# Performance work log

Measured on AMD Instinct MI355X. Metric: run time of the kernel, lower is better.

## Reference

```python
import jax, jax.numpy as jnp
import numpy as np

WS = 8   # window_size
SS = 4   # shift_size
NH = 12  # num_heads
DIM = 384
HD = DIM // NH


def _rel_index():
    coords = np.stack(np.meshgrid(np.arange(WS), np.arange(WS), indexing='ij'))  # (2, ws, ws)
    cf = coords.reshape(2, -1)                       # (2, n)
    rel = (cf[:, :, None] - cf[:, None, :]).transpose(1, 2, 0).copy()  # (n, n, 2)
    rel[..., 0] += WS - 1
    rel[..., 1] += WS - 1
    rel[..., 0] *= 2 * WS - 1
    return rel.sum(-1)                               # (n, n) int


def _attn_mask(h, w):
    img = np.zeros((h, w))
    sl = (slice(0, -WS), slice(-WS, -SS), slice(-SS, None))
    cnt = 0
    for hs in sl:
        for ws_ in sl:
            img[hs, ws_] = cnt
            cnt += 1
    mw = img.reshape(h // WS, WS, w // WS, WS).transpose(0, 2, 1, 3).reshape(-1, WS * WS)  # (nW, n)
    d = mw[:, None, :] - mw[:, :, None]
    return np.where(d != 0, -100.0, 0.0).astype(np.float32)  # (nW, n, n)


def setup_inputs() -> dict:
    key = jax.random.key(0)
    ks = jax.random.split(key, 10)
    B, H, W = 32, 64, 64
    std = 0.02
    return {
        'x': jax.random.normal(ks[0], (B, H, W, DIM), jnp.float32),
        'wq': jax.random.normal(ks[1], (DIM, DIM), jnp.float32) * std,
        'bq': jnp.zeros((DIM,), jnp.float32),
        'wk': jax.random.normal(ks[2], (DIM, DIM), jnp.float32) * std,
        'bk': jnp.zeros((DIM,), jnp.float32),
        'wv': jax.random.normal(ks[3], (DIM, DIM), jnp.float32) * std,
        'bv': jnp.zeros((DIM,), jnp.float32),
        'wo': jax.random.normal(ks[4], (DIM, DIM), jnp.float32) * std,
        'bo': jnp.zeros((DIM,), jnp.float32),
        'bias_table': jax.random.normal(ks[5], ((2 * WS - 1) ** 2, NH), jnp.float32) * std,
    }


def reference(x, wq, bq, wk, bk, wv, bv, wo, bo, bias_table):
    b, h, w, c = x.shape
    pad_h = (-h) % WS
    pad_w = (-w) % WS
    if pad_h or pad_w:
        x = jnp.pad(x, ((0, 0), (0, pad_h), (0, pad_w), (0, 0)))
    hp, wp = x.shape[1], x.shape[2]

    if SS > 0:
        x_sh = jnp.roll(x, shift=(-SS, -SS), axis=(1, 2))
        mask = jnp.asarray(_attn_mask(hp, wp))          # (nW, n, n)
    else:
        x_sh = x
        mask = None

    # window partition -> (B*nW, n, C)
    nwh, nww = hp // WS, wp // WS
    win = x_sh.reshape(b, nwh, WS, nww, WS, c).transpose(0, 1, 3, 2, 4, 5)
    win = win.reshape(-1, WS * WS, c)
    b_, n, _ = win.shape

    scale = HD ** -0.5
    q = (win @ wq.T + bq).reshape(b_, n, NH, HD).transpose(0, 2, 1, 3) * scale
    k = (win @ wk.T + bk).reshape(b_, n, NH, HD).transpose(0, 2, 1, 3)
    v = (win @ wv.T + bv).reshape(b_, n, NH, HD).transpose(0, 2, 1, 3)

    attn = jnp.einsum('bhnd,bhmd->bhnm', q, k)          # (b_, NH, n, n)
    rel = bias_table[jnp.asarray(_rel_index()).reshape(-1)].reshape(n, n, NH)
    attn = attn + rel.transpose(2, 0, 1)[None]
    if mask is not None:
        nW = mask.shape[0]
        attn = attn.reshape(b_ // nW, nW, NH, n, n) + mask[None, :, None]
        attn = attn.reshape(b_, NH, n, n)
    attn = jax.nn.softmax(attn, axis=-1)

    out = jnp.einsum('bhnm,bhmd->bhnd', attn, v).transpose(0, 2, 1, 3).reshape(b_, n, c)
    out = out @ wo.T + bo

    # window reverse -> (B, hp, wp, C)
    out = out.reshape(b, nwh, nww, WS, WS, c).transpose(0, 1, 3, 2, 4, 5).reshape(b, hp, wp, c)
    if SS > 0:
        out = jnp.roll(out, shift=(SS, SS), axis=(1, 2))
    return out[:, :h, :w, :]
```

## Files before the change

kernel.cpp:

```cpp
#include <hip/hip_runtime.h>
#include <hip/hip_bf16.h>

typedef short bf16x8 __attribute__((ext_vector_type(8)));
typedef float f32x4 __attribute__((ext_vector_type(4)));

#define NH_ 12
#define DIM_ 384

static __device__ __forceinline__ float bf2f_us(ushort u) {
    __hip_bfloat16 h; __builtin_memcpy(&h, &u, 2);
    return __bfloat162float(h);
}
static __device__ __forceinline__ ushort f2us(float f) {
    __hip_bfloat16 h = __float2bfloat16(f);
    ushort u; __builtin_memcpy(&u, &h, 2);
    return u;
}

static __device__ __forceinline__ void gload_lds16(const void* g, void* l) {
    __builtin_amdgcn_global_load_lds(
        (const __attribute__((address_space(1))) unsigned int*)g,
        (__attribute__((address_space(3))) unsigned int*)l, 16, 0, 0);
}

static __device__ __forceinline__ int regioncnt(int t, int wr, int wc) {
    int rr = (wr == 7) ? (((t >> 3) < 4) ? 1 : 2) : 0;
    int cc = (wc == 7) ? (((t & 7) < 4) ? 1 : 2) : 0;
    return rr * 3 + cc;
}

__global__ __launch_bounds__(256) void convert_kernel(
    const float* wq, const float* wk, const float* wv, const float* wo,
    const float* bq, const float* bk, const float* bv, const float* bo,
    const float* bt, ushort* __restrict__ dst)
{
    const int N = 594060;
    for (int i = blockIdx.x * 256 + threadIdx.x; i < N; i += gridDim.x * 256) {
        const float* src; int off;
        if (i < 589824) {
            int wsel = i / 147456; off = i - wsel * 147456;
            src = (wsel == 0) ? wq : (wsel == 1) ? wk : (wsel == 2) ? wv : wo;
        } else if (i < 591360) {
            int bsel = (i - 589824) / 384; off = (i - 589824) - bsel * 384;
            src = (bsel == 0) ? bq : (bsel == 1) ? bk : (bsel == 2) ? bv : bo;
        } else {
            off = i - 591360; src = bt;
        }
        dst[i] = f2us(src[off]);
    }
}

__global__ void bias_kernel(const ushort* __restrict__ tablec, float* __restrict__ biasmat) {
    int i = blockIdx.x;
    int j = threadIdx.x;
    int idx = ((i >> 3) - (j >> 3) + 7) * 15 + ((i & 7) - (j & 7) + 7);
    #pragma unroll
    for (int h = 0; h < NH_; ++h)
        biasmat[h * 4096 + i * 64 + j] = bf2f_us(tablec[idx * NH_ + h]);
}

__global__ __launch_bounds__(256, 3) void qkv_gemm(
    const float* __restrict__ x, const ushort* __restrict__ wb,
    ushort* __restrict__ qws, ushort* __restrict__ kws, ushort* __restrict__ vws,
    int wbase, int nmb)
{
    __shared__ __align__(16) ushort As[128 * 32];
    __shared__ __align__(16) ushort Bs[128 * 32];
    const int nwg = nmb * 9;
    const int orig = blockIdx.x;
    const int wgid = (orig & 7) * (nwg >> 3) + (orig >> 3);
    const int mb = wgid / 9, nt = wgid - mb * 9;
    const int wsel = nt / 3, ntm = nt - wsel * 3;
    const int n0 = nt * 128;
    const int tid = threadIdx.x, lane = tid & 63, wv = tid >> 6;
    const int col16 = lane & 15, quad = lane >> 4;
    const int wm = wv >> 1, wn = wv & 1;

    const float* arow[4];
    int lrs[4];
    #pragma unroll
    for (int it = 0; it < 4; ++it) {
        const int lr = (tid >> 3) + 32 * it;
        lrs[it] = lr;
        const int wglob = wbase + mb * 2 + (lr >> 6);
        const int token = lr & 63;
        const int b = wglob >> 6, widx = wglob & 63, wr = widx >> 3, wc = widx & 7;
        const int orr = (wr * 8 + (token >> 3) + 4) & 63;
        const int occ = (wc * 8 + (token & 7) + 4) & 63;
        arow[it] = x + (((size_t)b * 64 + orr) * 64 + occ) * DIM_ + (tid & 7) * 4;
    }

    f32x4 acc[4][4];
    #pragma unroll
    for (int i2 = 0; i2 < 4; ++i2)
        #pragma unroll
        for (int j2 = 0; j2 < 4; ++j2)
            acc[i2][j2] = (f32x4){0.f, 0.f, 0.f, 0.f};

    const ushort* bsrc = wb + (size_t)n0 * DIM_;
    const int srow = lane >> 2, scolb = (lane & 3) * 8;

    for (int kk = 0; kk < DIM_; kk += 32) {
        if (kk) __syncthreads();
        #pragma unroll
        for (int c2 = 0; c2 < 2; ++c2) {
            const int row = wv * 32 + c2 * 16 + srow;
            gload_lds16(bsrc + (size_t)row * DIM_ + kk + scolb, Bs + wv * 1024 + c2 * 512);
        }
        #pragma unroll
        for (int it = 0; it < 4; ++it) {
            const float4 v = *reinterpret_cast<const float4*>(arow[it] + kk);
            ushort4 u; u.x = f2us(v.x); u.y = f2us(v.y); u.z = f2us(v.z); u.w = f2us(v.w);
            *reinterpret_cast<ushort4*>(&As[lrs[it] * 32 + (tid & 7) * 4]) = u;
        }
        __syncthreads();
        bf16x8 af[4], bf[4];
        #pragma unroll
        for (int rt = 0; rt < 4; ++rt)
            af[rt] = *reinterpret_cast<const bf16x8*>(&As[(wm * 64 + rt * 16 + col16) * 32 + quad * 8]);
        #pragma unroll
        for (int ct = 0; ct < 4; ++ct)
            bf[ct] = *reinterpret_cast<const bf16x8*>(&Bs[(wn * 64 + ct * 16 + col16) * 32 + quad * 8]);
        #pragma unroll
        for (int rt = 0; rt < 4; ++rt)
            #pragma unroll
            for (int ct = 0; ct < 4; ++ct)
                acc[rt][ct] = __builtin_amdgcn_mfma_f32_16x16x32_bf16(af[rt], bf[ct], acc[rt][ct], 0, 0, 0);
    }

    const int lw = mb * 2 + wm;
    const float scale = 0.17677669529663687f;
    const ushort* bias_all = wb + 589824 + wsel * 384;
    #pragma unroll
    for (int ct = 0; ct < 4; ++ct) {
        const int jl = ntm * 128 + wn * 64 + ct * 16 + col16;
        const int head = jl >> 5, hd = jl & 31;
        const float bj = bf2f_us(bias_all[jl]);
        #pragma unroll
        for (int rt = 0; rt < 4; ++rt) {
            if (wsel == 2) {
                ushort4 pk;
                pk.x = f2us(acc[rt][ct][0] + bj);
                pk.y = f2us(acc[rt][ct][1] + bj);
                pk.z = f2us(acc[rt][ct][2] + bj);
                pk.w = f2us(acc[rt][ct][3] + bj);
                *reinterpret_cast<ushort4*>(
                    vws + ((size_t)(lw * NH_ + head) * 32 + hd) * 64 + rt * 16 + quad * 4) = pk;
            } else {
                #pragma unroll
                for (int r = 0; r < 4; ++r) {
                    const int token = rt * 16 + quad * 4 + r;
                    const float v = acc[rt][ct][r] + bj;
                    if (wsel == 0)
                        qws[((size_t)(lw * NH_ + head) * 64 + token) * 32 + hd] = f2us(v * scale);
                    else
                        kws[((size_t)(lw * NH_ + head) * 64 + token) * 32 + hd] = f2us(v);
                }
            }
        }
    }
}

__global__ __launch_bounds__(64) void attn_kernel(
    const __hip_bfloat16* __restrict__ qws, const __hip_bfloat16* __restrict__ kws,
    const __hip_bfloat16* __restrict__ vws, const float* __restrict__ biasmat,
    __hip_bfloat16* __restrict__ attnout, int wbase)
{
    __shared__ __align__(16) __hip_bfloat16 Pbuf[64 * 72];
    const int bid = blockIdx.x;
    const int lw = bid / NH_, h = bid - lw * NH_;
    const int w = wbase + lw;
    const int lane = threadIdx.x, col16 = lane & 15, quad = lane >> 4;
    const ushort* qp = reinterpret_cast<const ushort*>(qws) + ((size_t)lw * NH_ + h) * 64 * 32;
    const ushort* kp = reinterpret_cast<const ushort*>(kws) + ((size_t)lw * NH_ + h) * 64 * 32;
    const ushort* vp = reinterpret_cast<const ushort*>(vws) + ((size_t)lw * NH_ + h) * 32 * 64;

    bf16x8 aq[4], bk4[4];
    #pragma unroll
    for (int t = 0; t < 4; ++t) {
        aq[t]  = *reinterpret_cast<const bf16x8*>(qp + (t * 16 + col16) * 32 + quad * 8);
        bk4[t] = *reinterpret_cast<const bf16x8*>(kp + (t * 16 + col16) * 32 + quad * 8);
    }
    f32x4 S[4][4];
    #pragma unroll
    for (int rt = 0; rt < 4; ++rt) {
        #pragma unroll
        for (int ct = 0; ct < 4; ++ct) {
            f32x4 z = {0.f,0.f,0.f,0.f};
            S[rt][ct] = __builtin_amdgcn_mfma_f32_16x16x32_bf16(aq[rt], bk4[ct], z, 0, 0, 0);
        }
    }

    const int widx = w & 63, wr = widx >> 3, wc = widx & 7;
    #pragma unroll
    for (int ct = 0; ct < 4; ++ct) {
        const int jj = ct * 16 + col16;
        const int cntj = regioncnt(jj, wr, wc);
        #pragma unroll
        for (int rt = 0; rt < 4; ++rt) {
            #pragma unroll
            for (int r = 0; r < 4; ++r) {
                const int ii = rt * 16 + quad * 4 + r;
                float add = biasmat[h * 4096 + ii * 64 + jj];
                if (regioncnt(ii, wr, wc) != cntj) add -= 100.f;
                S[rt][ct][r] += add;
            }
        }
    }

    #pragma unroll
    for (int rt = 0; rt < 4; ++rt) {
        float rm[4], rs[4];
        #pragma unroll
        for (int r = 0; r < 4; ++r)
            rm[r] = fmaxf(fmaxf(S[rt][0][r], S[rt][1][r]), fmaxf(S[rt][2][r], S[rt][3][r]));
        #pragma unroll
        for (int d = 1; d <= 8; d <<= 1) {
            #pragma unroll
            for (int r = 0; r < 4; ++r) rm[r] = fmaxf(rm[r], __shfl_xor(rm[r], d, 64));
        }
        #pragma unroll
        for (int r = 0; r < 4; ++r) rs[r] = 0.f;
        #pragma unroll
        for (int ct = 0; ct < 4; ++ct) {
            #pragma unroll
            for (int r = 0; r < 4; ++r) {
                float p = __expf(S[rt][ct][r] - rm[r]);
                S[rt][ct][r] = p;
                rs[r] += p;
            }
        }
        #pragma unroll
        for (int d = 1; d <= 8; d <<= 1) {
            #pragma unroll
            for (int r = 0; r < 4; ++r) rs[r] += __shfl_xor(rs[r], d, 64);
        }
        #pragma unroll
        for (int ct = 0; ct < 4; ++ct) {
            #pragma unroll
            for (int r = 0; r < 4; ++r) {
                const float inv = 1.0f / rs[r];
                Pbuf[(rt * 16 + quad * 4 + r) * 72 + ct * 16 + col16] =
                    __float2bfloat16(S[rt][ct][r] * inv);
            }
        }
    }
    __syncthreads();

    f32x4 O[4][2];
    #pragma unroll
    for (int rt = 0; rt < 4; ++rt) {
        f32x4 z = {0.f,0.f,0.f,0.f};
        O[rt][0] = z; O[rt][1] = z;
    }
    const ushort* pb = reinterpret_cast<const ushort*>(Pbuf);
    #pragma unroll
    for (int ks = 0; ks < 2; ++ks) {
        bf16x8 bv0 = *reinterpret_cast<const bf16x8*>(vp + (col16)*64 + ks * 32 + quad * 8);
        bf16x8 bv1 = *reinterpret_cast<const bf16x8*>(vp + (16 + col16) * 64 + ks * 32 + quad * 8);
        #pragma unroll
        for (int rt = 0; rt < 4; ++rt) {
            bf16x8 ap = *reinterpret_cast<const bf16x8*>(pb + (rt * 16 + col16) * 72 + ks * 32 + quad * 8);
            O[rt][0] = __builtin_amdgcn_mfma_f32_16x16x32_bf16(ap, bv0, O[rt][0], 0, 0, 0);
            O[rt][1] = __builtin_amdgcn_mfma_f32_16x16x32_bf16(ap, bv1, O[rt][1], 0, 0, 0);
        }
    }
    __hip_bfloat16* op = attnout + (size_t)lw * 64 * DIM_ + h * 32;
    #pragma unroll
    for (int rt = 0; rt < 4; ++rt) {
        #pragma unroll
        for (int c2 = 0; c2 < 2; ++c2) {
            #pragma unroll
            for (int r = 0; r < 4; ++r) {
                const int token = rt * 16 + quad * 4 + r;
                op[token * DIM_ + c2 * 16 + col16] = __float2bfloat16(O[rt][c2][r]);
            }
        }
    }
}

__global__ __launch_bounds__(256, 3) void proj_gemm(
    const ushort* __restrict__ attnin, const ushort* __restrict__ wb,
    float* __restrict__ out, int wbase, int nmb)
{
    __shared__ __align__(16) ushort As[128 * 32];
    __shared__ __align__(16) ushort Bs[128 * 32];
    const int nwg = nmb * 3;
    const int orig = blockIdx.x;
    const int wgid = (orig & 7) * (nwg >> 3) + (orig >> 3);
    const int mb = wgid / 3, nt = wgid - mb * 3;
    const int n0 = nt * 128;
    const int tid = threadIdx.x, lane = tid & 63, wv = tid >> 6;
    const int col16 = lane & 15, quad = lane >> 4;
    const int wm = wv >> 1, wn = wv & 1;

    const ushort* asrc = attnin + (size_t)mb * 128 * DIM_;
    const ushort* bsrc = wb + (size_t)3 * 147456 + (size_t)n0 * DIM_;
    const int srow = lane >> 2, scolb = (lane & 3) * 8;

    f32x4 acc[4][4];
    #pragma unroll
    for (int i2 = 0; i2 < 4; ++i2)
        #pragma unroll
        for (int j2 = 0; j2 < 4; ++j2)
            acc[i2][j2] = (f32x4){0.f, 0.f, 0.f, 0.f};

    for (int kk = 0; kk < DIM_; kk += 32) {
        if (kk) __syncthreads();
        #pragma unroll
        for (int c2 = 0; c2 < 2; ++c2) {
            const int row = wv * 32 + c2 * 16 + srow;
            gload_lds16(asrc + (size_t)row * DIM_ + kk + scolb, As + wv * 1024 + c2 * 512);
            gload_lds16(bsrc + (size_t)row * DIM_ + kk + scolb, Bs + wv * 1024 + c2 * 512);
        }
        __syncthreads();
        bf16x8 af[4], bf[4];
        #pragma unroll
        for (int rt = 0; rt < 4; ++rt)
            af[rt] = *reinterpret_cast<const bf16x8*>(&As[(wm * 64 + rt * 16 + col16) * 32 + quad * 8]);
        #pragma unroll
        for (int ct = 0; ct < 4; ++ct)
            bf[ct] = *reinterpret_cast<const bf16x8*>(&Bs[(wn * 64 + ct * 16 + col16) * 32 + quad * 8]);
        #pragma unroll
        for (int rt = 0; rt < 4; ++rt)
            #pragma unroll
            for (int ct = 0; ct < 4; ++ct)
                acc[rt][ct] = __builtin_amdgcn_mfma_f32_16x16x32_bf16(af[rt], bf[ct], acc[rt][ct], 0, 0, 0);
    }

    const int lw = mb * 2 + wm;
    const int wglob = wbase + lw;
    const int b = wglob >> 6, widx = wglob & 63, wr = widx >> 3, wc = widx & 7;
    const ushort* boc = wb + 589824 + 3 * 384;
    #pragma unroll
    for (int ct = 0; ct < 4; ++ct) {
        const int j = n0 + wn * 64 + ct * 16 + col16;
        const float bj = bf2f_us(boc[j]);
        #pragma unroll
        for (int rt = 0; rt < 4; ++rt) {
            #pragma unroll
            for (int r = 0; r < 4; ++r) {
                const int token = rt * 16 + quad * 4 + r;
                const int orr = (wr * 8 + (token >> 3) + 4) & 63;
                const int occ = (wc * 8 + (token & 7) + 4) & 63;
                out[(((size_t)b * 64 + orr) * 64 + occ) * DIM_ + j] = acc[rt][ct][r] + bj;
            }
        }
    }
}

extern "C" void kernel_launch(void* const* d_in, const int* in_sizes, int n_in,
                              void* d_out, int out_size, void* d_ws, size_t ws_size,
                              hipStream_t stream) {
    const float* x = (const float*)d_in[0];
    float* out = (float*)d_out;
    char* ws = (char*)d_ws;

    ushort* wb      = (ushort*)ws;
    float*  biasmat = (float*)(ws + 1188352);
    const size_t FIXED = 1384960;

    int wchunk = 128;
    const int cands[4] = {2048, 1024, 512, 256};
    for (int i = 0; i < 4; ++i) {
        if (FIXED + (size_t)cands[i] * 4 * 49152 <= ws_size) { wchunk = cands[i]; break; }
    }
    const size_t CQ = (size_t)wchunk * NH_ * 64 * 32 * 2;
    __hip_bfloat16* qws = (__hip_bfloat16*)(ws + FIXED);
    __hip_bfloat16* kws = (__hip_bfloat16*)(ws + FIXED + CQ);
    __hip_bfloat16* vws = (__hip_bfloat16*)(ws + FIXED + 2 * CQ);
    __hip_bfloat16* att = (__hip_bfloat16*)(ws + FIXED + 3 * CQ);

    convert_kernel<<<dim3(512), dim3(256), 0, stream>>>(
        (const float*)d_in[1], (const float*)d_in[3], (const float*)d_in[5], (const float*)d_in[7],
        (const float*)d_in[2], (const float*)d_in[4], (const float*)d_in[6], (const float*)d_in[8],
        (const float*)d_in[9], wb);
    bias_kernel<<<dim3(64), dim3(64), 0, stream>>>(wb + 591360, biasmat);

    for (int c = 0; c < 2048 / wchunk; ++c) {
        const int wbase = c * wchunk;
        const int nmb = wchunk / 2;
        qkv_gemm<<<dim3(nmb * 9), dim3(256), 0, stream>>>(
            x, wb, (ushort*)qws, (ushort*)kws, (ushort*)vws, wbase, nmb);
        attn_kernel<<<dim3(wchunk * NH_), dim3(64), 0, stream>>>(qws, kws, vws, biasmat, att, wbase);
        proj_gemm<<<dim3(nmb * 3), dim3(256), 0, stream>>>(
            (const ushort*)att, wb, out, wbase, nmb);
    }
}
```

Measured before the change: 803.0 us.

## Double-buffer LDS tiles in QKV and projection GEMMs with fragment-ordered layout

```diff
diff --git a/kernel.cpp b/kernel.cpp
--- a/kernel.cpp
+++ b/kernel.cpp
@@ -59,13 +59,13 @@
         biasmat[h * 4096 + i * 64 + j] = bf2f_us(tablec[idx * NH_ + h]);
 }
 
-__global__ __launch_bounds__(256, 3) void qkv_gemm(
+__global__ __launch_bounds__(256, 4) void qkv_gemm(
     const float* __restrict__ x, const ushort* __restrict__ wb,
     ushort* __restrict__ qws, ushort* __restrict__ kws, ushort* __restrict__ vws,
     int wbase, int nmb)
 {
-    __shared__ __align__(16) ushort As[128 * 32];
-    __shared__ __align__(16) ushort Bs[128 * 32];
+    __shared__ __align__(16) ushort As[2][4096];
+    __shared__ __align__(16) ushort Bs[2][4096];
     const int nwg = nmb * 9;
     const int orig = blockIdx.x;
     const int wgid = (orig & 7) * (nwg >> 3) + (orig >> 3);
@@ -76,19 +76,22 @@
     const int col16 = lane & 15, quad = lane >> 4;
     const int wm = wv >> 1, wn = wv & 1;
 
+    const int kof = ((tid >> 1) & 3) * 8 + (tid & 1) * 4;
     const float* arow[4];
-    int lrs[4];
     #pragma unroll
     for (int it = 0; it < 4; ++it) {
-        const int lr = (tid >> 3) + 32 * it;
-        lrs[it] = lr;
-        const int wglob = wbase + mb * 2 + (lr >> 6);
-        const int token = lr & 63;
+        const int s = it * 128 + (tid >> 1);
+        const int row = (s >> 6) * 16 + ((s & 63) >> 2);
+        const int wglob = wbase + mb * 2 + (row >> 6);
+        const int token = row & 63;
         const int b = wglob >> 6, widx = wglob & 63, wr = widx >> 3, wc = widx & 7;
         const int orr = (wr * 8 + (token >> 3) + 4) & 63;
         const int occ = (wc * 8 + (token & 7) + 4) & 63;
-        arow[it] = x + (((size_t)b * 64 + orr) * 64 + occ) * DIM_ + (tid & 7) * 4;
-    }
+        arow[it] = x + (((size_t)b * 64 + orr) * 64 + occ) * DIM_ + kof;
+    }
+
+    const ushort* bsrc = wb + (size_t)n0 * DIM_;
+    const int brow_l = lane >> 2, bkof = (lane & 3) * 8;
 
     f32x4 acc[4][4];
     #pragma unroll
@@ -97,35 +100,60 @@
         for (int j2 = 0; j2 < 4; ++j2)
             acc[i2][j2] = (f32x4){0.f, 0.f, 0.f, 0.f};
 
-    const ushort* bsrc = wb + (size_t)n0 * DIM_;
-    const int srow = lane >> 2, scolb = (lane & 3) * 8;
-
-    for (int kk = 0; kk < DIM_; kk += 32) {
-        if (kk) __syncthreads();
-        #pragma unroll
-        for (int c2 = 0; c2 < 2; ++c2) {
-            const int row = wv * 32 + c2 * 16 + srow;
-            gload_lds16(bsrc + (size_t)row * DIM_ + kk + scolb, Bs + wv * 1024 + c2 * 512);
-        }
-        #pragma unroll
-        for (int it = 0; it < 4; ++it) {
-            const float4 v = *reinterpret_cast<const float4*>(arow[it] + kk);
-            ushort4 u; u.x = f2us(v.x); u.y = f2us(v.y); u.z = f2us(v.z); u.w = f2us(v.w);
-            *reinterpret_cast<ushort4*>(&As[lrs[it] * 32 + (tid & 7) * 4]) = u;
+    const int NK = DIM_ / 32;
+
+    #pragma unroll
+    for (int c2 = 0; c2 < 2; ++c2) {
+        const int blk = wv * 2 + c2;
+        gload_lds16(bsrc + (size_t)(blk * 16 + brow_l) * DIM_ + bkof, &Bs[0][blk * 512]);
+    }
+    #pragma unroll
+    for (int it = 0; it < 4; ++it) {
+        const float4 v = *reinterpret_cast<const float4*>(arow[it]);
+        ushort4 u4; u4.x = f2us(v.x); u4.y = f2us(v.y); u4.z = f2us(v.z); u4.w = f2us(v.w);
+        *reinterpret_cast<ushort4*>(&As[0][it * 1024 + tid * 4]) = u4;
+    }
+    __syncthreads();
+
+    for (int t = 0; t < NK; ++t) {
+        const int cur = t & 1, nxt = cur ^ 1;
+        const int kk = t * 32;
+        float4 av[4];
+        if (t + 1 < NK) {
+            #pragma unroll
+            for (int it = 0; it < 4; ++it)
+                av[it] = *reinterpret_cast<const float4*>(arow[it] + kk + 32);
+            #pragma unroll
+            for (int c2 = 0; c2 < 2; ++c2) {
+                const int blk = wv * 2 + c2;
+                gload_lds16(bsrc + (size_t)(blk * 16 + brow_l) * DIM_ + kk + 32 + bkof,
+                            &Bs[nxt][blk * 512]);
+            }
+        }
+        bf16x8 af[4], bfm[4];
+        #pragma unroll
+        for (int rt = 0; rt < 4; ++rt)
+            af[rt] = *reinterpret_cast<const bf16x8*>(
+                &As[cur][(wm * 4 + rt) * 512 + (col16 * 4 + quad) * 8]);
+        #pragma unroll
+        for (int ct = 0; ct < 4; ++ct)
+            bfm[ct] = *reinterpret_cast<const bf16x8*>(
+                &Bs[cur][(wn * 4 + ct) * 512 + (col16 * 4 + quad) * 8]);
+        #pragma unroll
+        for (int rt = 0; rt < 4; ++rt)
+            #pragma unroll
+            for (int ct = 0; ct < 4; ++ct)
+                acc[rt][ct] = __builtin_amdgcn_mfma_f32_16x16x32_bf16(af[rt], bfm[ct], acc[rt][ct], 0, 0, 0);
+        if (t + 1 < NK) {
+            #pragma unroll
+            for (int it = 0; it < 4; ++it) {
+                ushort4 u4;
+                u4.x = f2us(av[it].x); u4.y = f2us(av[it].y);
+                u4.z = f2us(av[it].z); u4.w = f2us(av[it].w);
+                *reinterpret_cast<ushort4*>(&As[nxt][it * 1024 + tid * 4]) = u4;
+            }
         }
         __syncthreads();
-        bf16x8 af[4], bf[4];
-        #pragma unroll
-        for (int rt = 0; rt < 4; ++rt)
-            af[rt] = *reinterpret_cast<const bf16x8*>(&As[(wm * 64 + rt * 16 + col16) * 32 + quad * 8]);
-        #pragma unroll
-        for (int ct = 0; ct < 4; ++ct)
-            bf[ct] = *reinterpret_cast<const bf16x8*>(&Bs[(wn * 64 + ct * 16 + col16) * 32 + quad * 8]);
-        #pragma unroll
-        for (int rt = 0; rt < 4; ++rt)
-            #pragma unroll
-            for (int ct = 0; ct < 4; ++ct)
-                acc[rt][ct] = __builtin_amdgcn_mfma_f32_16x16x32_bf16(af[rt], bf[ct], acc[rt][ct], 0, 0, 0);
     }
 
     const int lw = mb * 2 + wm;
@@ -279,12 +307,12 @@
     }
 }
 
-__global__ __launch_bounds__(256, 3) void proj_gemm(
+__global__ __launch_bounds__(256, 4) void proj_gemm(
     const ushort* __restrict__ attnin, const ushort* __restrict__ wb,
     float* __restrict__ out, int wbase, int nmb)
 {
-    __shared__ __align__(16) ushort As[128 * 32];
-    __shared__ __align__(16) ushort Bs[128 * 32];
+    __shared__ __align__(16) ushort As[2][4096];
+    __shared__ __align__(16) ushort Bs[2][4096];
     const int nwg = nmb * 3;
     const int orig = blockIdx.x;
     const int wgid = (orig & 7) * (nwg >> 3) + (orig >> 3);
@@ -296,7 +324,7 @@
 
     const ushort* asrc = attnin + (size_t)mb * 128 * DIM_;
     const ushort* bsrc = wb + (size_t)3 * 147456 + (size_t)n0 * DIM_;
-    const int srow = lane >> 2, scolb = (lane & 3) * 8;
+    const int row_l = lane >> 2, kof_l = (lane & 3) * 8;
 
     f32x4 acc[4][4];
     #pragma unroll
@@ -305,27 +333,44 @@
         for (int j2 = 0; j2 < 4; ++j2)
             acc[i2][j2] = (f32x4){0.f, 0.f, 0.f, 0.f};
 
-    for (int kk = 0; kk < DIM_; kk += 32) {
-        if (kk) __syncthreads();
-        #pragma unroll
-        for (int c2 = 0; c2 < 2; ++c2) {
-            const int row = wv * 32 + c2 * 16 + srow;
-            gload_lds16(asrc + (size_t)row * DIM_ + kk + scolb, As + wv * 1024 + c2 * 512);
-            gload_lds16(bsrc + (size_t)row * DIM_ + kk + scolb, Bs + wv * 1024 + c2 * 512);
-        }
+    const int NK = DIM_ / 32;
+
+    #pragma unroll
+    for (int c2 = 0; c2 < 2; ++c2) {
+        const int blk = wv * 2 + c2;
+        gload_lds16(asrc + (size_t)(blk * 16 + row_l) * DIM_ + kof_l, &As[0][blk * 512]);
+        gload_lds16(bsrc + (size_t)(blk * 16 + row_l) * DIM_ + kof_l, &Bs[0][blk * 512]);
+    }
+    __syncthreads();
+
+    for (int t = 0; t < NK; ++t) {
+        const int cur = t & 1, nxt = cur ^ 1;
+        const int kk = t * 32;
+        if (t + 1 < NK) {
+            #pragma unroll
+            for (int c2 = 0; c2 < 2; ++c2) {
+                const int blk = wv * 2 + c2;
+                gload_lds16(asrc + (size_t)(blk * 16 + row_l) * DIM_ + kk + 32 + kof_l,
+                            &As[nxt][blk * 512]);
+                gload_lds16(bsrc + (size_t)(blk * 16 + row_l) * DIM_ + kk + 32 + kof_l,
+                            &Bs[nxt][blk * 512]);
+            }
+        }
+        bf16x8 af[4], bfm[4];
+        #pragma unroll
+        for (int rt = 0; rt < 4; ++rt)
+            af[rt] = *reinterpret_cast<const bf16x8*>(
+                &As[cur][(wm * 4 + rt) * 512 + (col16 * 4 + quad) * 8]);
+        #pragma unroll
+        for (int ct = 0; ct < 4; ++ct)
+            bfm[ct] = *reinterpret_cast<const bf16x8*>(
+                &Bs[cur][(wn * 4 + ct) * 512 + (col16 * 4 + quad) * 8]);
+        #pragma unroll
+        for (int rt = 0; rt < 4; ++rt)
+            #pragma unroll
+            for (int ct = 0; ct < 4; ++ct)
+                acc[rt][ct] = __builtin_amdgcn_mfma_f32_16x16x32_bf16(af[rt], bfm[ct], acc[rt][ct], 0, 0, 0);
         __syncthreads();
-        bf16x8 af[4], bf[4];
-        #pragma unroll
-        for (int rt = 0; rt < 4; ++rt)
-            af[rt] = *reinterpret_cast<const bf16x8*>(&As[(wm * 64 + rt * 16 + col16) * 32 + quad * 8]);
-        #pragma unroll
-        for (int ct = 0; ct < 4; ++ct)
-            bf[ct] = *reinterpret_cast<const bf16x8*>(&Bs[(wn * 64 + ct * 16 + col16) * 32 + quad * 8]);
-        #pragma unroll
-        for (int rt = 0; rt < 4; ++rt)
-            #pragma unroll
-            for (int ct = 0; ct < 4; ++ct)
-                acc[rt][ct] = __builtin_amdgcn_mfma_f32_16x16x32_bf16(af[rt], bf[ct], acc[rt][ct], 0, 0, 0);
     }
 
     const int lw = mb * 2 + wm;
```

Result: faster. 777.6 us (-3.2%).
